# Kernel tuning notes

Hardware: AMD Instinct MI355X
Metric: run time of the kernel (lower is better)

The kernel has to match this reference:

```python
import jax, jax.numpy as jnp
import numpy as np

N = 50000      # nodes
E = 600000     # edges
P = 200000     # prediction edges
IN = 128       # in_channels
HID = 128      # hidden per head
H1, H2 = 4, 2  # heads
BN_EPS = 1e-5
NEG_SLOPE = 0.2


def _rn(k, shape, scale=0.05):
    return jax.random.normal(k, shape, jnp.float32) * scale


def setup_inputs() -> dict:
    key = jax.random.key(0)
    ks = jax.random.split(key, 24)
    inp = {}
    inp['x'] = jax.random.normal(ks[0], (N, IN), jnp.float32)
    inp['ei'] = jax.random.randint(ks[1], (2, E), 0, N, dtype=jnp.int32)
    inp['pred_edges'] = jax.random.randint(ks[2], (2, P), 0, N, dtype=jnp.int32)
    inp['pert'] = jax.random.normal(ks[3], (N,), jnp.float32)
    inp['pr'] = jax.random.uniform(ks[4], (N,), jnp.float32)
    # GATv2 layer 1: in=IN -> H1 heads x HID
    inp['Wl1'] = _rn(ks[5], (IN, H1 * HID))
    inp['bl1'] = jnp.zeros((H1 * HID,), jnp.float32)
    inp['Wr1'] = _rn(ks[6], (IN, H1 * HID))
    inp['br1'] = jnp.zeros((H1 * HID,), jnp.float32)
    inp['att1'] = _rn(ks[7], (H1, HID))
    inp['bias1'] = jnp.zeros((H1 * HID,), jnp.float32)
    # BatchNorm1d(H1*HID) eval-mode params
    inp['bn1_g'] = jnp.ones((H1 * HID,), jnp.float32)
    inp['bn1_b'] = jnp.zeros((H1 * HID,), jnp.float32)
    inp['bn1_m'] = _rn(ks[8], (H1 * HID,))
    inp['bn1_v'] = jax.random.uniform(ks[9], (H1 * HID,), jnp.float32, 0.5, 1.5)
    # GATv2 layer 2: in=H1*HID -> H2 heads x HID
    inp['Wl2'] = _rn(ks[10], (H1 * HID, H2 * HID))
    inp['bl2'] = jnp.zeros((H2 * HID,), jnp.float32)
    inp['Wr2'] = _rn(ks[11], (H1 * HID, H2 * HID))
    inp['br2'] = jnp.zeros((H2 * HID,), jnp.float32)
    inp['att2'] = _rn(ks[12], (H2, HID))
    inp['bias2'] = jnp.zeros((H2 * HID,), jnp.float32)
    inp['bn2_g'] = jnp.ones((H2 * HID,), jnp.float32)
    inp['bn2_b'] = jnp.zeros((H2 * HID,), jnp.float32)
    inp['bn2_m'] = _rn(ks[13], (H2 * HID,))
    inp['bn2_v'] = jax.random.uniform(ks[14], (H2 * HID,), jnp.float32, 0.5, 1.5)
    # proj: Linear(H2*HID*2 + 2 + 1, 2)
    inp['Wp'] = _rn(ks[15], (H2 * HID * 2 + 3, 2))
    inp['bp'] = jnp.zeros((2,), jnp.float32)
    return inp


def gatv2(x, src, dst, Wl, bl, Wr, br, att, bias, n):
    """GATv2Conv (concat=True): e_ij = att . LeakyReLU(xl_j + xr_i), segment softmax over dst."""
    H, C = att.shape
    xl = (x @ Wl + bl).reshape(n, H, C)
    xr = (x @ Wr + br).reshape(n, H, C)
    e = jax.nn.leaky_relu(xl[src] + xr[dst], NEG_SLOPE)     # [E, H, C]
    score = jnp.einsum('ehc,hc->eh', e, att)                 # [E, H]
    m = jax.ops.segment_max(score, dst, num_segments=n)     # [N, H]
    ex = jnp.exp(score - m[dst])
    denom = jax.ops.segment_sum(ex, dst, num_segments=n)
    alpha = ex / denom[dst]                                  # [E, H]
    out = jax.ops.segment_sum(alpha[:, :, None] * xl[src], dst, num_segments=n)
    return out.reshape(n, H * C) + bias


def batchnorm_eval(h, g, b, m, v):
    return (h - m) * jax.lax.rsqrt(v + BN_EPS) * g + b


def reference(x, ei, pred_edges, pert, pr,
              Wl1, bl1, Wr1, br1, att1, bias1, bn1_g, bn1_b, bn1_m, bn1_v,
              Wl2, bl2, Wr2, br2, att2, bias2, bn2_g, bn2_b, bn2_m, bn2_v,
              Wp, bp):
    n = x.shape[0]
    loop = jnp.arange(n, dtype=ei.dtype)                    # add_self_loops=True
    src = jnp.concatenate([ei[0], loop])
    dst = jnp.concatenate([ei[1], loop])
    h = gatv2(x, src, dst, Wl1, bl1, Wr1, br1, att1, bias1, n)
    h = jax.nn.relu(batchnorm_eval(h, bn1_g, bn1_b, bn1_m, bn1_v))
    h = gatv2(h, src, dst, Wl2, bl2, Wr2, br2, att2, bias2, n)
    z = jax.nn.relu(batchnorm_eval(h, bn2_g, bn2_b, bn2_m, bn2_v))
    s, d = pred_edges[0], pred_edges[1]
    feat = jnp.concatenate([z[s], z[d], pr[s][:, None], pr[d][:, None],
                            (pert[s] * pert[d])[:, None]], axis=1)
    return feat @ Wp + bp
```

## Files before the change

### kernel.cpp

```cpp
#include <hip/hip_runtime.h>
#include <math.h>

#define BN_EPS 1e-5f
#define N_NODES 50000
#define E_EDGES 600000

typedef __attribute__((ext_vector_type(8))) short bf16x8;
typedef __attribute__((ext_vector_type(4))) short bf16x4;
typedef __attribute__((ext_vector_type(4))) float f32x4;

__device__ __forceinline__ short f2bf(float f) {
    unsigned u = __float_as_uint(f);
    u += 0x7fffu + ((u >> 16) & 1u);
    return (short)(u >> 16);
}
__device__ __forceinline__ float bf2f(short s) {
    return __uint_as_float(((unsigned)(unsigned short)s) << 16);
}

__device__ short g_xlb[(size_t)N_NODES * 512];
__device__ short g_xrb[(size_t)N_NODES * 512];
__device__ short g_h1b[(size_t)N_NODES * 512];
__device__ short g_xb[(size_t)N_NODES * 128];
__device__ short g_zb[(size_t)N_NODES * 256];
__device__ short g_wt[393216];
__device__ int   g_rowptr[N_NODES + 1];
__device__ int   g_bsum[256];
__device__ int   g_cursor[N_NODES];
__device__ int   g_counts[N_NODES];
__device__ int   g_csrc[E_EDGES + N_NODES];


__global__ void k_init_counts(int* __restrict__ counts, int n) {
    int i = blockIdx.x * blockDim.x + threadIdx.x;
    if (i < n) counts[i] = 1;
}

__global__ void k_hist(const int* __restrict__ ei, int E, int* __restrict__ counts) {
    int e = blockIdx.x * blockDim.x + threadIdx.x;
    if (e < E) atomicAdd(&counts[ei[E + e]], 1);
}

__global__ void k_scan1(const int* __restrict__ counts, int n,
                        int* __restrict__ rp, int* __restrict__ bsum) {
    __shared__ int sd[256];
    int t = threadIdx.x;
    int g = blockIdx.x * 256 + t;
    int v = (g < n) ? counts[g] : 0;
    sd[t] = v;
    __syncthreads();
    for (int o = 1; o < 256; o <<= 1) {
        int u = (t >= o) ? sd[t - o] : 0;
        __syncthreads();
        sd[t] += u;
        __syncthreads();
    }
    if (g < n) rp[g + 1] = sd[t];
    if (t == 255) bsum[blockIdx.x] = sd[255];
}

__global__ void k_scan2(int* __restrict__ bsum, int nb) {
    __shared__ int sd[256];
    int t = threadIdx.x;
    int v = (t < nb) ? bsum[t] : 0;
    sd[t] = v;
    __syncthreads();
    for (int o = 1; o < 256; o <<= 1) {
        int u = (t >= o) ? sd[t - o] : 0;
        __syncthreads();
        sd[t] += u;
        __syncthreads();
    }
    if (t < nb) bsum[t] = sd[t] - v;
}

__global__ void k_scan3(int* __restrict__ rp, const int* __restrict__ bsum, int n) {
    int g = blockIdx.x * blockDim.x + threadIdx.x;
    if (g < n) rp[g + 1] += bsum[g >> 8];
    if (g == 0) rp[0] = 0;
}

__global__ void k_fill(const int* __restrict__ rp, int* __restrict__ cursor,
                       int* __restrict__ csrc, int n) {
    int i = blockIdx.x * blockDim.x + threadIdx.x;
    if (i < n) {
        int p = rp[i];
        csrc[p] = i;
        cursor[i] = p + 1;
    }
}

__global__ void k_scatter(const int* __restrict__ ei, int E,
                          int* __restrict__ cursor, int* __restrict__ csrc) {
    int e = blockIdx.x * blockDim.x + threadIdx.x;
    if (e < E) {
        int d = ei[E + e];
        int p = atomicAdd(&cursor[d], 1);
        csrc[p] = ei[e];
    }
}


__global__ void k_f32_to_bf16_v4(const float* __restrict__ in, short* __restrict__ out,
                                 int n4) {
    int i = blockIdx.x * blockDim.x + threadIdx.x;
    if (i < n4) {
        float4 v = ((const float4*)in)[i];
        short4 o;
        o.x = f2bf(v.x); o.y = f2bf(v.y); o.z = f2bf(v.z); o.w = f2bf(v.w);
        ((short4*)out)[i] = o;
    }
}

__global__ void k_transpose_w(const float* __restrict__ W, short* __restrict__ Wt,
                              int K, int N) {
    __shared__ float s[32][33];
    int n0 = blockIdx.x * 32, k0 = blockIdx.y * 32;
    int tx = threadIdx.x, ty = threadIdx.y;
    #pragma unroll
    for (int q = 0; q < 4; q++)
        s[ty * 4 + q][tx] = W[(size_t)(k0 + ty * 4 + q) * N + n0 + tx];
    __syncthreads();
    #pragma unroll
    for (int q = 0; q < 4; q++)
        Wt[(size_t)(n0 + ty * 4 + q) * K + k0 + tx] = f2bf(s[tx][ty * 4 + q]);
}

__global__ __launch_bounds__(256) void k_gemm_dual(
    const short* __restrict__ A, const short* __restrict__ Bt,
    const float* __restrict__ bias_l, const float* __restrict__ bias_r,
    short* __restrict__ Cl, short* __restrict__ Cr,
    int M, int N, int K)
{
    __shared__ short sA[128][68];
    __shared__ short sB0[128][68];
    __shared__ short sB1[128][68];
    int tid = threadIdx.x;
    int wid = tid >> 6, lane = tid & 63;
    int m0 = blockIdx.y * 128;
    int n0 = blockIdx.x * 256;
    int wr = (wid >> 1) * 64;
    int wc = (wid & 1) * 64;
    f32x4 acc0[4][4] = {};
    f32x4 acc1[4][4] = {};

    for (int k0 = 0; k0 < K; k0 += 64) {
        #pragma unroll
        for (int i = 0; i < 4; i++) {
            int c = tid + i * 256;
            int r = c >> 3;
            int col = (c & 7) * 8;
            bf16x8 v = {};
            int gr = m0 + r;
            if (gr < M) v = *(const bf16x8*)(A + (size_t)gr * K + k0 + col);
            *(bf16x8*)&sA[r][col] = v;
            bf16x8 b0 = *(const bf16x8*)(Bt + (size_t)(n0 + r) * K + k0 + col);
            *(bf16x8*)&sB0[r][col] = b0;
            bf16x8 b1 = *(const bf16x8*)(Bt + (size_t)(n0 + 128 + r) * K + k0 + col);
            *(bf16x8*)&sB1[r][col] = b1;
        }
        __syncthreads();
        #pragma unroll
        for (int kk = 0; kk < 2; kk++) {
            bf16x8 af[4], bf0[4], bf1[4];
            #pragma unroll
            for (int i = 0; i < 4; i++)
                af[i] = *(bf16x8*)&sA[wr + i * 16 + (lane & 15)][kk * 32 + (lane >> 4) * 8];
            #pragma unroll
            for (int j = 0; j < 4; j++) {
                bf0[j] = *(bf16x8*)&sB0[wc + j * 16 + (lane & 15)][kk * 32 + (lane >> 4) * 8];
                bf1[j] = *(bf16x8*)&sB1[wc + j * 16 + (lane & 15)][kk * 32 + (lane >> 4) * 8];
            }
            #pragma unroll
            for (int i = 0; i < 4; i++)
                #pragma unroll
                for (int j = 0; j < 4; j++) {
                    acc0[i][j] = __builtin_amdgcn_mfma_f32_16x16x32_bf16(
                        bf0[j], af[i], acc0[i][j], 0, 0, 0);
                    acc1[i][j] = __builtin_amdgcn_mfma_f32_16x16x32_bf16(
                        bf1[j], af[i], acc1[i][j], 0, 0, 0);
                }
        }
        __syncthreads();
    }
    short* outp;
    const float* bp2;
    int cb;
    if (n0 < N) { outp = Cl; bp2 = bias_l; cb = n0; }
    else        { outp = Cr; bp2 = bias_r; cb = n0 - N; }
    #pragma unroll
    for (int i = 0; i < 4; i++) {
        int rowg = m0 + wr + i * 16 + (lane & 15);
        if (rowg >= M) continue;
        #pragma unroll
        for (int j = 0; j < 4; j++) {
            int nl = cb + wc + j * 16 + (lane >> 4) * 4;
            float4 b0 = *(const float4*)(bp2 + nl);
            float4 b1 = *(const float4*)(bp2 + nl + 128);
            short o0[4], o1[4];
            o0[0] = f2bf(acc0[i][j][0] + b0.x); o0[1] = f2bf(acc0[i][j][1] + b0.y);
            o0[2] = f2bf(acc0[i][j][2] + b0.z); o0[3] = f2bf(acc0[i][j][3] + b0.w);
            o1[0] = f2bf(acc1[i][j][0] + b1.x); o1[1] = f2bf(acc1[i][j][1] + b1.y);
            o1[2] = f2bf(acc1[i][j][2] + b1.z); o1[3] = f2bf(acc1[i][j][3] + b1.w);
            *(bf16x4*)(outp + (size_t)rowg * N + nl)       = *(bf16x4*)o0;
            *(bf16x4*)(outp + (size_t)rowg * N + nl + 128) = *(bf16x4*)o1;
        }
    }
}

template <int H, typename OT>
__global__ void k_gat_agg(const short* __restrict__ xl, const short* __restrict__ xr,
                          const float* __restrict__ att,
                          const int* __restrict__ rp, const int* __restrict__ csrc,
                          const float* __restrict__ bias,
                          const float* __restrict__ bng, const float* __restrict__ bnb,
                          const float* __restrict__ bnm, const float* __restrict__ bnv,
                          OT* __restrict__ out, int n) {
    constexpr int G = 64 / H;
    constexpr int CPL = 128 / G;
    const int D = H * 128;
    int wid = (blockIdx.x * blockDim.x + threadIdx.x) >> 6;
    int lane = threadIdx.x & 63;
    if (wid >= n) return;
    const int i = wid;
    const int h = lane / G;
    const int ch0 = h * 128 + (lane % G) * CPL;

    float xrv[CPL], attv[CPL];
    {
        short raw[CPL];
        if constexpr (CPL == 8)
            *(bf16x8*)raw = *(const bf16x8*)(xr + (size_t)i * D + ch0);
        else
            *(bf16x4*)raw = *(const bf16x4*)(xr + (size_t)i * D + ch0);
        #pragma unroll
        for (int q = 0; q < CPL; q++) {
            xrv[q] = bf2f(raw[q]);
            attv[q] = att[ch0 + q];
        }
    }
    float m = -INFINITY, dnm = 0.f, acc[CPL] = {};

    int e0 = rp[i], e1 = rp[i + 1];
    int e = e0;
    for (; e + 1 < e1; e += 2) {
        int j0 = csrc[e], j1 = csrc[e + 1];
        float xlv0[CPL], xlv1[CPL];
        {
            short r0[CPL], r1[CPL];
            if constexpr (CPL == 8) {
                *(bf16x8*)r0 = *(const bf16x8*)(xl + (size_t)j0 * D + ch0);
                *(bf16x8*)r1 = *(const bf16x8*)(xl + (size_t)j1 * D + ch0);
            } else {
                *(bf16x4*)r0 = *(const bf16x4*)(xl + (size_t)j0 * D + ch0);
                *(bf16x4*)r1 = *(const bf16x4*)(xl + (size_t)j1 * D + ch0);
            }
            #pragma unroll
            for (int q = 0; q < CPL; q++) { xlv0[q] = bf2f(r0[q]); xlv1[q] = bf2f(r1[q]); }
        }
        float p0 = 0.f, p1 = 0.f;
        #pragma unroll
        for (int q = 0; q < CPL; q++) {
            float v0 = xlv0[q] + xrv[q];
            float v1 = xlv1[q] + xrv[q];
            v0 = fmaxf(v0, 0.2f * v0);
            v1 = fmaxf(v1, 0.2f * v1);
            p0 = fmaf(attv[q], v0, p0);
            p1 = fmaf(attv[q], v1, p1);
        }
        #pragma unroll
        for (int o = G / 2; o > 0; o >>= 1) {
            p0 += __shfl_xor(p0, o, 64);
            p1 += __shfl_xor(p1, o, 64);
        }
        float mn = fmaxf(m, fmaxf(p0, p1));
        float scale = __expf(m - mn);
        float w0 = __expf(p0 - mn);
        float w1 = __expf(p1 - mn);
        dnm = dnm * scale + w0 + w1;
        #pragma unroll
        for (int q = 0; q < CPL; q++)
            acc[q] = fmaf(w1, xlv1[q], fmaf(w0, xlv0[q], acc[q] * scale));
        m = mn;
    }
    if (e < e1) {
        int j = csrc[e];
        float xlv[CPL];
        {
            short raw[CPL];
            if constexpr (CPL == 8)
                *(bf16x8*)raw = *(const bf16x8*)(xl + (size_t)j * D + ch0);
            else
                *(bf16x4*)raw = *(const bf16x4*)(xl + (size_t)j * D + ch0);
            #pragma unroll
            for (int q = 0; q < CPL; q++) xlv[q] = bf2f(raw[q]);
        }
        float part = 0.f;
        #pragma unroll
        for (int q = 0; q < CPL; q++) {
            float v = xlv[q] + xrv[q];
            v = fmaxf(v, 0.2f * v);
            part = fmaf(attv[q], v, part);
        }
        #pragma unroll
        for (int o = G / 2; o > 0; o >>= 1) part += __shfl_xor(part, o, 64);
        float mn = fmaxf(m, part);
        float scale = __expf(m - mn);
        float p = __expf(part - mn);
        dnm = dnm * scale + p;
        #pragma unroll
        for (int q = 0; q < CPL; q++) acc[q] = fmaf(p, xlv[q], acc[q] * scale);
        m = mn;
    }

    float inv = 1.f / dnm;
    float res[CPL];
    #pragma unroll
    for (int q = 0; q < CPL; q++) {
        int ch = ch0 + q;
        float o = acc[q] * inv + bias[ch];
        float vv = (o - bnm[ch]) * rsqrtf(bnv[ch] + BN_EPS) * bng[ch] + bnb[ch];
        res[q] = fmaxf(vv, 0.f);
    }
    if constexpr (sizeof(OT) == 2) {
        short ov[CPL];
        #pragma unroll
        for (int q = 0; q < CPL; q++) ov[q] = f2bf(res[q]);
        if constexpr (CPL == 8)
            *(bf16x8*)(out + (size_t)i * D + ch0) = *(bf16x8*)ov;
        else
            *(bf16x4*)(out + (size_t)i * D + ch0) = *(bf16x4*)ov;
    } else {
        #pragma unroll
        for (int q = 0; q < CPL; q++) out[(size_t)i * D + ch0 + q] = res[q];
    }
}

__global__ void k_pred(const short* __restrict__ z, const int* __restrict__ pe,
                       const float* __restrict__ pr, const float* __restrict__ pert,
                       const float* __restrict__ Wp, const float* __restrict__ bp,
                       float* __restrict__ out, int P) {
    int wid = (blockIdx.x * blockDim.x + threadIdx.x) >> 6;
    int lane = threadIdx.x & 63;
    if (wid >= P) return;
    int s = pe[wid], d = pe[P + wid];
    int node = (lane < 32) ? s : d;
    int off = (lane & 31) * 8;
    short raw[8];
    *(bf16x8*)raw = *(const bf16x8*)(z + (size_t)node * 256 + off);
    int fbase = (lane < 32) ? off : 256 + off;
    float a0 = 0.f, a1 = 0.f;
    #pragma unroll
    for (int q = 0; q < 8; q++) {
        float v = bf2f(raw[q]);
        a0 = fmaf(v, Wp[(fbase + q) * 2 + 0], a0);
        a1 = fmaf(v, Wp[(fbase + q) * 2 + 1], a1);
    }
    #pragma unroll
    for (int o = 32; o > 0; o >>= 1) {
        a0 += __shfl_xor(a0, o, 64);
        a1 += __shfl_xor(a1, o, 64);
    }
    if (lane == 0) {
        float prs = pr[s], prd = pr[d], pp = pert[s] * pert[d];
        a0 += prs * Wp[512 * 2 + 0] + prd * Wp[513 * 2 + 0] + pp * Wp[514 * 2 + 0] + bp[0];
        a1 += prs * Wp[512 * 2 + 1] + prd * Wp[513 * 2 + 1] + pp * Wp[514 * 2 + 1] + bp[1];
        *(float2*)(out + (size_t)wid * 2) = make_float2(a0, a1);
    }
}


extern "C" void kernel_launch(void* const* d_in, const int* in_sizes, int n_in,
                              void* d_out, int out_size, void* d_ws, size_t ws_size,
                              hipStream_t stream) {
    const float* x    = (const float*)d_in[0];
    const int*   ei   = (const int*)d_in[1];
    const int*   pe   = (const int*)d_in[2];
    const float* pert = (const float*)d_in[3];
    const float* pr   = (const float*)d_in[4];
    const float* Wl1  = (const float*)d_in[5];
    const float* bl1  = (const float*)d_in[6];
    const float* Wr1  = (const float*)d_in[7];
    const float* br1  = (const float*)d_in[8];
    const float* att1 = (const float*)d_in[9];
    const float* bias1= (const float*)d_in[10];
    const float* bn1g = (const float*)d_in[11];
    const float* bn1b = (const float*)d_in[12];
    const float* bn1m = (const float*)d_in[13];
    const float* bn1v = (const float*)d_in[14];
    const float* Wl2  = (const float*)d_in[15];
    const float* bl2  = (const float*)d_in[16];
    const float* Wr2  = (const float*)d_in[17];
    const float* br2  = (const float*)d_in[18];
    const float* att2 = (const float*)d_in[19];
    const float* bias2= (const float*)d_in[20];
    const float* bn2g = (const float*)d_in[21];
    const float* bn2b = (const float*)d_in[22];
    const float* bn2m = (const float*)d_in[23];
    const float* bn2v = (const float*)d_in[24];
    const float* Wp   = (const float*)d_in[25];
    const float* bp   = (const float*)d_in[26];

    const int n  = in_sizes[3];
    const int E  = in_sizes[1] / 2;
    const int P  = in_sizes[2] / 2;
    const int IN = in_sizes[0] / n;
    const int D1 = 512, D2 = 256;

    static short* xlb = nullptr;
    static short* xrb = nullptr;
    static short* h1b = nullptr;
    static short* xb  = nullptr;
    static short* zb  = nullptr;
    static short* wt  = nullptr;
    static int *rowptr = nullptr, *bsum = nullptr, *cursor = nullptr,
               *counts = nullptr, *csrc = nullptr;
    if (!xlb) {
        hipGetSymbolAddress((void**)&xlb,    HIP_SYMBOL(g_xlb));
        hipGetSymbolAddress((void**)&xrb,    HIP_SYMBOL(g_xrb));
        hipGetSymbolAddress((void**)&h1b,    HIP_SYMBOL(g_h1b));
        hipGetSymbolAddress((void**)&xb,     HIP_SYMBOL(g_xb));
        hipGetSymbolAddress((void**)&zb,     HIP_SYMBOL(g_zb));
        hipGetSymbolAddress((void**)&wt,     HIP_SYMBOL(g_wt));
        hipGetSymbolAddress((void**)&rowptr, HIP_SYMBOL(g_rowptr));
        hipGetSymbolAddress((void**)&bsum,   HIP_SYMBOL(g_bsum));
        hipGetSymbolAddress((void**)&cursor, HIP_SYMBOL(g_cursor));
        hipGetSymbolAddress((void**)&counts, HIP_SYMBOL(g_counts));
        hipGetSymbolAddress((void**)&csrc,   HIP_SYMBOL(g_csrc));
    }

    short* xl1b = xlb;
    short* xr1b = xrb;
    short* xl2b = xlb;
    short* xr2b = xlb + (size_t)n * D2;
    short* WtL1 = wt;
    short* WtL2 = wt + 131072;
    short* Wl1t = wt;
    short* Wr1t = wt + 65536;
    short* Wl2t = wt + 131072;
    short* Wr2t = wt + 262144;

    const int nb = (n + 255) / 256;

    k_init_counts<<<nb, 256, 0, stream>>>(counts, n);
    k_hist<<<(E + 255) / 256, 256, 0, stream>>>(ei, E, counts);
    k_scan1<<<nb, 256, 0, stream>>>(counts, n, rowptr, bsum);
    k_scan2<<<1, 256, 0, stream>>>(bsum, nb);
    k_scan3<<<nb, 256, 0, stream>>>(rowptr, bsum, n);
    k_fill<<<nb, 256, 0, stream>>>(rowptr, cursor, csrc, n);
    k_scatter<<<(E + 255) / 256, 256, 0, stream>>>(ei, E, cursor, csrc);

    {
        int n4 = n * IN / 4;
        k_f32_to_bf16_v4<<<(n4 + 255) / 256, 256, 0, stream>>>(x, xb, n4);
        k_transpose_w<<<dim3(D1 / 32, IN / 32), dim3(32, 8), 0, stream>>>(Wl1, Wl1t, IN, D1);
        k_transpose_w<<<dim3(D1 / 32, IN / 32), dim3(32, 8), 0, stream>>>(Wr1, Wr1t, IN, D1);
        k_transpose_w<<<dim3(D2 / 32, D1 / 32), dim3(32, 8), 0, stream>>>(Wl2, Wl2t, D1, D2);
        k_transpose_w<<<dim3(D2 / 32, D1 / 32), dim3(32, 8), 0, stream>>>(Wr2, Wr2t, D1, D2);
    }

    const int mb = (n + 127) / 128;

    k_gemm_dual<<<dim3(2 * D1 / 256, mb), 256, 0, stream>>>(
        xb, WtL1, bl1, br1, xl1b, xr1b, n, D1, IN);
    k_gat_agg<4, short><<<(n + 3) / 4, 256, 0, stream>>>(xl1b, xr1b, att1, rowptr, csrc,
                                                  bias1, bn1g, bn1b, bn1m, bn1v, h1b, n);
    k_gemm_dual<<<dim3(2 * D2 / 256, mb), 256, 0, stream>>>(
        h1b, WtL2, bl2, br2, xl2b, xr2b, n, D2, D1);
    k_gat_agg<2, short><<<(n + 3) / 4, 256, 0, stream>>>(xl2b, xr2b, att2, rowptr, csrc,
                                                  bias2, bn2g, bn2b, bn2m, bn2v, zb, n);
    k_pred<<<(P + 3) / 4, 256, 0, stream>>>(zb, pe, pr, pert, Wp, bp,
                                            (float*)d_out, P);
}
```

Measured before the change: 625.8 us.

## Use direct global-to-LDS loads with XOR swizzle in GEMM and unroll aggregation by four

The dual GEMM now loads its tiles with global_load_lds straight into unpadded shared memory, using an XOR swizzle in place of padding to avoid bank conflicts. Buffers are padded to a multiple of 128 rows so the row bounds checks can be dropped. The GAT aggregation loop handles four edges per step instead of two, which puts more independent gathers in flight at the cost of more registers. The padded rows past N are read uninitialized and their outputs are written but never used.

After: 617.5 us. About the same (-1.3%).

```diff
diff --git a/kernel.cpp b/kernel.cpp
--- a/kernel.cpp
+++ b/kernel.cpp
@@ -3,6 +3,7 @@
 
 #define BN_EPS 1e-5f
 #define N_NODES 50000
+#define M_PAD   50048
 #define E_EDGES 600000
 
 typedef __attribute__((ext_vector_type(8))) short bf16x8;
@@ -17,12 +18,16 @@
 __device__ __forceinline__ float bf2f(short s) {
     return __uint_as_float(((unsigned)(unsigned short)s) << 16);
 }
-
-__device__ short g_xlb[(size_t)N_NODES * 512];
-__device__ short g_xrb[(size_t)N_NODES * 512];
-__device__ short g_h1b[(size_t)N_NODES * 512];
-__device__ short g_xb[(size_t)N_NODES * 128];
-__device__ short g_zb[(size_t)N_NODES * 256];
+__device__ __forceinline__ void gload_lds16(const short* g, short* l) {
+    __builtin_amdgcn_global_load_lds((const __attribute__((address_space(1))) void*)g,
+                                     (__attribute__((address_space(3))) void*)l, 16, 0, 0);
+}
+
+__device__ short g_xlb[(size_t)M_PAD * 512];
+__device__ short g_xrb[(size_t)M_PAD * 512];
+__device__ short g_h1b[(size_t)M_PAD * 512];
+__device__ short g_xb[(size_t)M_PAD * 128];
+__device__ short g_zb[(size_t)M_PAD * 256];
 __device__ short g_wt[393216];
 __device__ int   g_rowptr[N_NODES + 1];
 __device__ int   g_bsum[256];
@@ -130,46 +135,51 @@
     const short* __restrict__ A, const short* __restrict__ Bt,
     const float* __restrict__ bias_l, const float* __restrict__ bias_r,
     short* __restrict__ Cl, short* __restrict__ Cr,
-    int M, int N, int K)
+    int N, int K)
 {
-    __shared__ short sA[128][68];
-    __shared__ short sB0[128][68];
-    __shared__ short sB1[128][68];
+    __shared__ short sA[128][64];
+    __shared__ short sB0[128][64];
+    __shared__ short sB1[128][64];
     int tid = threadIdx.x;
     int wid = tid >> 6, lane = tid & 63;
     int m0 = blockIdx.y * 128;
     int n0 = blockIdx.x * 256;
     int wr = (wid >> 1) * 64;
     int wc = (wid & 1) * 64;
+    int rowL = wid * 32 + (lane >> 3);
+    int chunk = lane & 7;
+
     f32x4 acc0[4][4] = {};
     f32x4 acc1[4][4] = {};
 
     for (int k0 = 0; k0 < K; k0 += 64) {
         #pragma unroll
         for (int i = 0; i < 4; i++) {
-            int c = tid + i * 256;
-            int r = c >> 3;
-            int col = (c & 7) * 8;
-            bf16x8 v = {};
-            int gr = m0 + r;
-            if (gr < M) v = *(const bf16x8*)(A + (size_t)gr * K + k0 + col);
-            *(bf16x8*)&sA[r][col] = v;
-            bf16x8 b0 = *(const bf16x8*)(Bt + (size_t)(n0 + r) * K + k0 + col);
-            *(bf16x8*)&sB0[r][col] = b0;
-            bf16x8 b1 = *(const bf16x8*)(Bt + (size_t)(n0 + 128 + r) * K + k0 + col);
-            *(bf16x8*)&sB1[r][col] = b1;
+            int row = rowL + i * 8;
+            int cs = chunk ^ (row & 7);
+            const short* ga = A  + ((size_t)(m0 + row) * K + k0 + cs * 8);
+            const short* g0 = Bt + ((size_t)(n0 + row) * K + k0 + cs * 8);
+            const short* g1 = Bt + ((size_t)(n0 + 128 + row) * K + k0 + cs * 8);
+            gload_lds16(ga, &sA[wid * 32 + i * 8][0]);
+            gload_lds16(g0, &sB0[wid * 32 + i * 8][0]);
+            gload_lds16(g1, &sB1[wid * 32 + i * 8][0]);
         }
         __syncthreads();
         #pragma unroll
         for (int kk = 0; kk < 2; kk++) {
             bf16x8 af[4], bf0[4], bf1[4];
             #pragma unroll
-            for (int i = 0; i < 4; i++)
-                af[i] = *(bf16x8*)&sA[wr + i * 16 + (lane & 15)][kk * 32 + (lane >> 4) * 8];
+            for (int i = 0; i < 4; i++) {
+                int r = wr + i * 16 + (lane & 15);
+                int c = ((kk * 4 + (lane >> 4)) ^ (r & 7)) << 3;
+                af[i] = *(bf16x8*)&sA[r][c];
+            }
             #pragma unroll
             for (int j = 0; j < 4; j++) {
-                bf0[j] = *(bf16x8*)&sB0[wc + j * 16 + (lane & 15)][kk * 32 + (lane >> 4) * 8];
-                bf1[j] = *(bf16x8*)&sB1[wc + j * 16 + (lane & 15)][kk * 32 + (lane >> 4) * 8];
+                int r = wc + j * 16 + (lane & 15);
+                int c = ((kk * 4 + (lane >> 4)) ^ (r & 7)) << 3;
+                bf0[j] = *(bf16x8*)&sB0[r][c];
+                bf1[j] = *(bf16x8*)&sB1[r][c];
             }
             #pragma unroll
             for (int i = 0; i < 4; i++)
@@ -191,7 +201,6 @@
     #pragma unroll
     for (int i = 0; i < 4; i++) {
         int rowg = m0 + wr + i * 16 + (lane & 15);
-        if (rowg >= M) continue;
         #pragma unroll
         for (int j = 0; j < 4; j++) {
             int nl = cb + wc + j * 16 + (lane >> 4) * 4;
@@ -243,47 +252,60 @@
 
     int e0 = rp[i], e1 = rp[i + 1];
     int e = e0;
-    for (; e + 1 < e1; e += 2) {
-        int j0 = csrc[e], j1 = csrc[e + 1];
-        float xlv0[CPL], xlv1[CPL];
+    for (; e + 3 < e1; e += 4) {
+        int j0 = csrc[e], j1 = csrc[e + 1], j2 = csrc[e + 2], j3 = csrc[e + 3];
+        float x0[CPL], x1[CPL], x2[CPL], x3[CPL];
         {
-            short r0[CPL], r1[CPL];
+            short r0[CPL], r1[CPL], r2[CPL], r3[CPL];
             if constexpr (CPL == 8) {
                 *(bf16x8*)r0 = *(const bf16x8*)(xl + (size_t)j0 * D + ch0);
                 *(bf16x8*)r1 = *(const bf16x8*)(xl + (size_t)j1 * D + ch0);
+                *(bf16x8*)r2 = *(const bf16x8*)(xl + (size_t)j2 * D + ch0);
+                *(bf16x8*)r3 = *(const bf16x8*)(xl + (size_t)j3 * D + ch0);
             } else {
                 *(bf16x4*)r0 = *(const bf16x4*)(xl + (size_t)j0 * D + ch0);
                 *(bf16x4*)r1 = *(const bf16x4*)(xl + (size_t)j1 * D + ch0);
+                *(bf16x4*)r2 = *(const bf16x4*)(xl + (size_t)j2 * D + ch0);
+                *(bf16x4*)r3 = *(const bf16x4*)(xl + (size_t)j3 * D + ch0);
             }
             #pragma unroll
-            for (int q = 0; q < CPL; q++) { xlv0[q] = bf2f(r0[q]); xlv1[q] = bf2f(r1[q]); }
-        }
-        float p0 = 0.f, p1 = 0.f;
+            for (int q = 0; q < CPL; q++) {
+                x0[q] = bf2f(r0[q]); x1[q] = bf2f(r1[q]);
+                x2[q] = bf2f(r2[q]); x3[q] = bf2f(r3[q]);
+            }
+        }
+        float p0 = 0.f, p1 = 0.f, p2 = 0.f, p3 = 0.f;
         #pragma unroll
         for (int q = 0; q < CPL; q++) {
-            float v0 = xlv0[q] + xrv[q];
-            float v1 = xlv1[q] + xrv[q];
-            v0 = fmaxf(v0, 0.2f * v0);
-            v1 = fmaxf(v1, 0.2f * v1);
-            p0 = fmaf(attv[q], v0, p0);
-            p1 = fmaf(attv[q], v1, p1);
+            float v0 = x0[q] + xrv[q], v1 = x1[q] + xrv[q];
+            float v2 = x2[q] + xrv[q], v3 = x3[q] + xrv[q];
+            v0 = fmaxf(v0, 0.2f * v0); v1 = fmaxf(v1, 0.2f * v1);
+            v2 = fmaxf(v2, 0.2f * v2); v3 = fmaxf(v3, 0.2f * v3);
+            p0 = fmaf(attv[q], v0, p0); p1 = fmaf(attv[q], v1, p1);
+            p2 = fmaf(attv[q], v2, p2); p3 = fmaf(attv[q], v3, p3);
         }
         #pragma unroll
         for (int o = G / 2; o > 0; o >>= 1) {
             p0 += __shfl_xor(p0, o, 64);
             p1 += __shfl_xor(p1, o, 64);
-        }
-        float mn = fmaxf(m, fmaxf(p0, p1));
+            p2 += __shfl_xor(p2, o, 64);
+            p3 += __shfl_xor(p3, o, 64);
+        }
+        float mn = fmaxf(fmaxf(fmaxf(p0, p1), fmaxf(p2, p3)), m);
         float scale = __expf(m - mn);
-        float w0 = __expf(p0 - mn);
-        float w1 = __expf(p1 - mn);
-        dnm = dnm * scale + w0 + w1;
-        #pragma unroll
-        for (int q = 0; q < CPL; q++)
-            acc[q] = fmaf(w1, xlv1[q], fmaf(w0, xlv0[q], acc[q] * scale));
+        float w0 = __expf(p0 - mn), w1 = __expf(p1 - mn);
+        float w2 = __expf(p2 - mn), w3 = __expf(p3 - mn);
+        dnm = dnm * scale + (w0 + w1) + (w2 + w3);
+        #pragma unroll
+        for (int q = 0; q < CPL; q++) {
+            float a = fmaf(w0, x0[q], acc[q] * scale);
+            a = fmaf(w1, x1[q], a);
+            a = fmaf(w2, x2[q], a);
+            acc[q] = fmaf(w3, x3[q], a);
+        }
         m = mn;
     }
-    if (e < e1) {
+    for (; e < e1; e++) {
         int j = csrc[e];
         float xlv[CPL];
         {
@@ -432,7 +454,7 @@
     short* xl1b = xlb;
     short* xr1b = xrb;
     short* xl2b = xlb;
-    short* xr2b = xlb + (size_t)n * D2;
+    short* xr2b = xlb + (size_t)M_PAD * D2;
     short* WtL1 = wt;
     short* WtL2 = wt + 131072;
     short* Wl1t = wt;
@@ -459,14 +481,14 @@
         k_transpose_w<<<dim3(D2 / 32, D1 / 32), dim3(32, 8), 0, stream>>>(Wr2, Wr2t, D1, D2);
     }
 
-    const int mb = (n + 127) / 128;
+    const int mb = M_PAD / 128;
 
     k_gemm_dual<<<dim3(2 * D1 / 256, mb), 256, 0, stream>>>(
-        xb, WtL1, bl1, br1, xl1b, xr1b, n, D1, IN);
+        xb, WtL1, bl1, br1, xl1b, xr1b, D1, IN);
     k_gat_agg<4, short><<<(n + 3) / 4, 256, 0, stream>>>(xl1b, xr1b, att1, rowptr, csrc,
                                                   bias1, bn1g, bn1b, bn1m, bn1v, h1b, n);
     k_gemm_dual<<<dim3(2 * D2 / 256, mb), 256, 0, stream>>>(
-        h1b, WtL2, bl2, br2, xl2b, xr2b, n, D2, D1);
+        h1b, WtL2, bl2, br2, xl2b, xr2b, D2, D1);
     k_gat_agg<2, short><<<(n + 3) / 4, 256, 0, stream>>>(xl2b, xr2b, att2, rowptr, csrc,
                                                   bias2, bn2g, bn2b, bn2m, bn2v, zb, n);
     k_pred<<<(P + 3) / 4, 256, 0, stream>>>(zb, pe, pr, pert, Wp, bp,
```
